# Kernel optimization log

Hardware: AMD Instinct MI355X
Metric: run time of the kernel (lower is better)

## Reference

```python
import jax, jax.numpy as jnp
import numpy as np

N_NODES = 100000
HIDDEN = 128
N_EDGES = 1000000


def setup_inputs() -> dict:
    key = jax.random.key(0)
    k1, k2, k3 = jax.random.split(key, 3)
    z = jax.random.normal(k1, (N_NODES, HIDDEN), dtype=jnp.float32)
    edge_index = jax.random.randint(k2, (2, N_EDGES), 0, N_NODES, dtype=jnp.int64)
    # xavier_uniform for square matrix: bound = sqrt(6/(fan_in+fan_out))
    bound = float(np.sqrt(6.0 / (HIDDEN + HIDDEN)))
    weights = jax.random.uniform(k3, (HIDDEN, HIDDEN), dtype=jnp.float32,
                                 minval=-bound, maxval=bound)
    return {"z": z, "edge_index": edge_index, "weights": weights}


def reference(z, edge_index, weights):
    # symm=True: symmetrize the bilinear form
    W = weights + weights.T                      # [d, d]
    z_src = z[edge_index[0]]                     # [E, d] gather
    z_dst = z[edge_index[1]]                     # [E, d] gather
    # torch: (W @ z_dst.T).T == z_dst @ W.T
    value = jnp.einsum('ed,dk,ek->e', z_src, W, z_dst)  # row-wise bilinear score
    return jax.nn.sigmoid(value)
```

## Files before the change

### kernel.cpp

```cpp
#include <hip/hip_runtime.h>

#define HIDDEN 128
#define BSHIFT 10
#define NBMAX 128
#define CAP 10752

typedef _Float16 f16;
typedef f16 f16x2 __attribute__((ext_vector_type(2)));
typedef f16 f16x4 __attribute__((ext_vector_type(4)));
typedef f16 f16x8 __attribute__((ext_vector_type(8)));
typedef float f32x16 __attribute__((ext_vector_type(16)));
typedef unsigned long long ull;
typedef ull ull2 __attribute__((ext_vector_type(2)));

static __device__ __forceinline__ float fdot2(f16x2 a, f16x2 b, float c) {
    return __builtin_amdgcn_fdot2(a, b, c, false);
}

static __device__ __forceinline__ int widx(int j, int x) {
    return j * HIDDEN + ((((x >> 3) + (j & 7)) & 15) << 3) + (x & 7);
}

static __device__ __forceinline__ void build_w(f16* wlt, const float* __restrict__ w) {
    int tid = threadIdx.x;
    #pragma unroll 4
    for (int it = 0; it < 16; ++it) {
        int idx4 = it * 256 + tid;
        int n = idx4 >> 5, k0 = (idx4 & 31) * 4;
        float4 wv = *(const float4*)&w[n * HIDDEN + k0];
        f16x4 v = {(f16)wv.x, (f16)wv.y, (f16)wv.z, (f16)wv.w};
        *(f16x4*)&wlt[widx(n, k0)] = v;
    }
    __syncthreads();
    for (int kk = 0; kk < 33; ++kk) {
        int i = kk * 256 + tid;
        if (i < 8256) {
            int k = i >> 7, r = i & 127;
            if (k == 0) {
                int e = widx(r, r);
                f16 a = wlt[e];
                wlt[e] = a + a;
            } else {
                int c = (r + k) & 127;
                int ea = widx(r, c), eb = widx(c, r);
                f16 a = wlt[ea], b = wlt[eb];
                f16 s = a + b;
                wlt[ea] = s; wlt[eb] = s;
            }
        }
    }
    __syncthreads();
}

__global__ __launch_bounds__(256, 4) void gemm_scatter(const float* __restrict__ z,
                                                       const float* __restrict__ w,
                                                       f16* __restrict__ zh,
                                                       f16* __restrict__ uh,
                                                       const int* __restrict__ eidx,
                                                       int* __restrict__ cursor,
                                                       ull* __restrict__ perm,
                                                       int nrows, int E, int nb, int ngemm) {
    __shared__ f16 wlt[HIDDEN * HIDDEN];
    int tid = threadIdx.x;

    if (blockIdx.x >= ngemm) {
        int* lh    = (int*)wlt;
        int* lbase = lh + NBMAX;
        int base = (blockIdx.x - ngemm) * 4096;
        if (tid < NBMAX) lh[tid] = 0;
        __syncthreads();
        int s[16], d[16], bb[16];
        #pragma unroll
        for (int i = 0; i < 16; ++i) {
            int e = base + i * 256 + tid;
            bb[i] = -1;
            if (e < E) {
                s[i] = eidx[e]; d[i] = eidx[E + e];
                int b = d[i] >> BSHIFT;
                int r = atomicAdd(&lh[b], 1);
                bb[i] = b | (r << 7);
            }
        }
        __syncthreads();
        if (tid < nb && lh[tid]) lbase[tid] = atomicAdd(&cursor[tid], lh[tid]);
        __syncthreads();
        #pragma unroll
        for (int i = 0; i < 16; ++i) {
            if (bb[i] >= 0) {
                int e = base + i * 256 + tid;
                int b = bb[i] & 127, r = bb[i] >> 7;
                unsigned pib = ((unsigned)(lbase[b] + r)) % CAP;
                ull v = (ull)s[i] | ((ull)d[i] << 17) | ((ull)(e + 1) << 34);
                perm[(long)b * CAP + pib] = v;
            }
        }
        return;
    }

    build_w(wlt, w);

    int wave = tid >> 6, lane = tid & 63;
    int row0 = blockIdx.x * 128 + wave * 32;
    if (row0 > nrows - 32) row0 = nrows - 32;

    int m = lane & 31, half = lane >> 5;
    int rot = m & 7;
    const float* zr = z  + (size_t)(row0 + m) * HIDDEN + half * 8;
    f16*        zhr = zh + (size_t)(row0 + m) * HIDDEN + half * 8;
    const f16* wrow = &wlt[m * HIDDEN];

    f32x16 acc0, acc1, acc2, acc3;
    #pragma unroll
    for (int r = 0; r < 16; ++r) { acc0[r] = 0.f; acc1[r] = 0.f; acc2[r] = 0.f; acc3[r] = 0.f; }

    #pragma unroll
    for (int ks = 0; ks < 8; ++ks) {
        float4 a0 = *(const float4*)(zr + 16 * ks);
        float4 a1 = *(const float4*)(zr + 16 * ks + 4);
        f16x8 af = {(f16)a0.x, (f16)a0.y, (f16)a0.z, (f16)a0.w,
                    (f16)a1.x, (f16)a1.y, (f16)a1.z, (f16)a1.w};
        *(f16x8*)(zhr + 16 * ks) = af;
        int c = ((half + 2 * ks + rot) & 15) << 3;
        f16x8 b0 = *(const f16x8*)&wrow[c];
        f16x8 b1 = *(const f16x8*)&wrow[32 * HIDDEN + c];
        f16x8 b2 = *(const f16x8*)&wrow[64 * HIDDEN + c];
        f16x8 b3 = *(const f16x8*)&wrow[96 * HIDDEN + c];
        acc0 = __builtin_amdgcn_mfma_f32_32x32x16_f16(af, b0, acc0, 0, 0, 0);
        acc1 = __builtin_amdgcn_mfma_f32_32x32x16_f16(af, b1, acc1, 0, 0, 0);
        acc2 = __builtin_amdgcn_mfma_f32_32x32x16_f16(af, b2, acc2, 0, 0, 0);
        acc3 = __builtin_amdgcn_mfma_f32_32x32x16_f16(af, b3, acc3, 0, 0, 0);
    }

    f16* ur = uh + (size_t)row0 * HIDDEN;
    #pragma unroll
    for (int r = 0; r < 16; ++r) {
        int row = (r & 3) + 8 * (r >> 2) + 4 * half;
        f16* p = ur + (size_t)row * HIDDEN + m;
        p[0]  = (f16)acc0[r];
        p[32] = (f16)acc1[r];
        p[64] = (f16)acc2[r];
        p[96] = (f16)acc3[r];
    }
}

static __device__ __forceinline__ void score_edge(const f16* uh, const f16* zh,
                                                  ull p, float* out, int t, int E) {
    int src = (int)(p & 0x1FFFF);
    int dst = (int)((p >> 17) & 0x1FFFF);
    int ep  = (int)(p >> 34);
    const float4* a4 = (const float4*)(uh + (size_t)src * HIDDEN);
    const float4* b4 = (const float4*)(zh + (size_t)dst * HIDDEN);
    float4 av = a4[t], bv = b4[t];
    const f16x2* ap = (const f16x2*)&av;
    const f16x2* bp = (const f16x2*)&bv;
    float s = 0.f;
    #pragma unroll
    for (int i = 0; i < 4; ++i) s = fdot2(ap[i], bp[i], s);
    #pragma unroll
    for (int off = 8; off > 0; off >>= 1) s += __shfl_down(s, off, 16);
    if (t == 0 && ep > 0 && ep <= E) out[ep - 1] = 1.0f / (1.0f + __expf(-s));
}

__global__ __launch_bounds__(256, 8) void edge_bin(const f16* __restrict__ uh,
                                                   const f16* __restrict__ zh,
                                                   const ull* __restrict__ perm,
                                                   float* __restrict__ out,
                                                   int E, int cpx) {
    int tid = threadIdx.x;
    int g = tid >> 4, t = tid & 15;
    int b = blockIdx.x;
    int chunk = (b & 7) * cpx + (b >> 3);
    long slot = (long)chunk * 32 + g * 2;
    ull2 p = *(const ull2*)&perm[slot];

    int src0 = (int)(p.x & 0x1FFFF), dst0 = (int)((p.x >> 17) & 0x1FFFF), e0 = (int)(p.x >> 34);
    int src1 = (int)(p.y & 0x1FFFF), dst1 = (int)((p.y >> 17) & 0x1FFFF), e1 = (int)(p.y >> 34);

    float4 a0 = ((const float4*)(uh + (size_t)src0 * HIDDEN))[t];
    float4 b0 = ((const float4*)(zh + (size_t)dst0 * HIDDEN))[t];
    float4 a1 = ((const float4*)(uh + (size_t)src1 * HIDDEN))[t];
    float4 b1 = ((const float4*)(zh + (size_t)dst1 * HIDDEN))[t];

    const f16x2* ap0 = (const f16x2*)&a0; const f16x2* bp0 = (const f16x2*)&b0;
    const f16x2* ap1 = (const f16x2*)&a1; const f16x2* bp1 = (const f16x2*)&b1;
    float s0 = 0.f, s1 = 0.f;
    #pragma unroll
    for (int i = 0; i < 4; ++i) {
        s0 = fdot2(ap0[i], bp0[i], s0);
        s1 = fdot2(ap1[i], bp1[i], s1);
    }
    #pragma unroll
    for (int off = 8; off > 0; off >>= 1) {
        s0 += __shfl_xor(s0, off, 16);
        s1 += __shfl_xor(s1, off, 16);
    }
    float sv = (t == 0) ? s0 : s1;
    int   ev = (t == 0) ? e0 : e1;
    if (t < 2 && ev > 0 && ev <= E) out[ev - 1] = 1.0f / (1.0f + __expf(-sv));
}

__global__ __launch_bounds__(256, 4) void gemm_only(const float* __restrict__ z,
                                                    const float* __restrict__ w,
                                                    f16* __restrict__ zh,
                                                    f16* __restrict__ uh, int nrows) {
    __shared__ f16 wlt[HIDDEN * HIDDEN];
    int tid = threadIdx.x;
    build_w(wlt, w);

    int wave = tid >> 6, lane = tid & 63;
    int row0 = blockIdx.x * 128 + wave * 32;
    if (row0 > nrows - 32) row0 = nrows - 32;
    int m = lane & 31, half = lane >> 5;
    int rot = m & 7;
    const float* zr = z  + (size_t)(row0 + m) * HIDDEN + half * 8;
    f16*        zhr = zh + (size_t)(row0 + m) * HIDDEN + half * 8;
    const f16* wrow = &wlt[m * HIDDEN];
    f32x16 acc0, acc1, acc2, acc3;
    #pragma unroll
    for (int r = 0; r < 16; ++r) { acc0[r] = 0.f; acc1[r] = 0.f; acc2[r] = 0.f; acc3[r] = 0.f; }
    #pragma unroll
    for (int ks = 0; ks < 8; ++ks) {
        float4 a0 = *(const float4*)(zr + 16 * ks);
        float4 a1 = *(const float4*)(zr + 16 * ks + 4);
        f16x8 af = {(f16)a0.x, (f16)a0.y, (f16)a0.z, (f16)a0.w,
                    (f16)a1.x, (f16)a1.y, (f16)a1.z, (f16)a1.w};
        *(f16x8*)(zhr + 16 * ks) = af;
        int c = ((half + 2 * ks + rot) & 15) << 3;
        f16x8 b0 = *(const f16x8*)&wrow[c];
        f16x8 b1 = *(const f16x8*)&wrow[32 * HIDDEN + c];
        f16x8 b2 = *(const f16x8*)&wrow[64 * HIDDEN + c];
        f16x8 b3 = *(const f16x8*)&wrow[96 * HIDDEN + c];
        acc0 = __builtin_amdgcn_mfma_f32_32x32x16_f16(af, b0, acc0, 0, 0, 0);
        acc1 = __builtin_amdgcn_mfma_f32_32x32x16_f16(af, b1, acc1, 0, 0, 0);
        acc2 = __builtin_amdgcn_mfma_f32_32x32x16_f16(af, b2, acc2, 0, 0, 0);
        acc3 = __builtin_amdgcn_mfma_f32_32x32x16_f16(af, b3, acc3, 0, 0, 0);
    }
    f16* ur = uh + (size_t)row0 * HIDDEN;
    #pragma unroll
    for (int r = 0; r < 16; ++r) {
        int row = (r & 3) + 8 * (r >> 2) + 4 * half;
        f16* p = ur + (size_t)row * HIDDEN + m;
        p[0]  = (f16)acc0[r];
        p[32] = (f16)acc1[r];
        p[64] = (f16)acc2[r];
        p[96] = (f16)acc3[r];
    }
}

__global__ __launch_bounds__(256) void edge_score16(const f16* __restrict__ uh,
                                                    const f16* __restrict__ zh,
                                                    const int* __restrict__ eidx,
                                                    float* __restrict__ out, int E) {
    int tid = threadIdx.x;
    int g = tid >> 4, t = tid & 15;
    int e = blockIdx.x * 16 + g;
    if (e >= E) return;
    ull p = (ull)eidx[e] | ((ull)eidx[E + e] << 17) | ((ull)(e + 1) << 34);
    score_edge(uh, zh, p, out, t, E);
}

extern "C" void kernel_launch(void* const* d_in, const int* in_sizes, int n_in,
                              void* d_out, int out_size, void* d_ws, size_t ws_size,
                              hipStream_t stream) {
    const float* z    = (const float*)d_in[0];
    const int*   eidx = (const int*)d_in[1];
    const float* w    = (const float*)d_in[2];
    float* out = (float*)d_out;

    int nrows = in_sizes[0] / HIDDEN;
    int E = out_size;
    int nb = (nrows >> BSHIFT) + 1;

    f16* zh     = (f16*)d_ws;
    f16* uh     = zh + (size_t)nrows * HIDDEN;
    int* cursor = (int*)(uh + (size_t)nrows * HIDDEN);
    ull* perm   = (ull*)(cursor + NBMAX + 4);

    long nslots = (long)nb * CAP;
    size_t need = (size_t)((char*)(perm + nslots) - (char*)d_ws);
    bool binned = ws_size >= need;

    int ngemm = (nrows + 127) / 128;
    int nscat = (E + 4095) / 4096;

    if (binned) {
        gemm_scatter<<<ngemm + nscat, 256, 0, stream>>>(z, w, zh, uh, eidx, cursor,
                                                        perm, nrows, E, nb, ngemm);
        long ngrp = nslots / 32;
        int cpx = (int)(ngrp / 8);
        edge_bin<<<(int)ngrp, 256, 0, stream>>>(uh, zh, perm, out, E, cpx);
    } else {
        gemm_only<<<ngemm, 256, 0, stream>>>(z, w, zh, uh, nrows);
        edge_score16<<<(E + 15) / 16, 256, 0, stream>>>(uh, zh, eidx, out, E);
    }
}
```

Measured before the change: 161.4 us.

## Precompute symmetrized fp16 W in a prep kernel and process two row tiles per block

A small prep kernel now builds the symmetrized, transposed fp16 weight matrix once into workspace. GEMM blocks copy it into LDS with vectorized loads instead of each block redoing the symmetrization with two barrier phases. Each GEMM block also handles 256 rows (two 128-row tiles), which halves the GEMM block count and spreads the W setup cost over more rows. The price is one extra kernel launch and fewer GEMM blocks for parallelism.

```diff
diff --git a/kernel.cpp b/kernel.cpp
--- a/kernel.cpp
+++ b/kernel.cpp
@@ -7,7 +7,6 @@
 
 typedef _Float16 f16;
 typedef f16 f16x2 __attribute__((ext_vector_type(2)));
-typedef f16 f16x4 __attribute__((ext_vector_type(4)));
 typedef f16 f16x8 __attribute__((ext_vector_type(8)));
 typedef float f32x16 __attribute__((ext_vector_type(16)));
 typedef unsigned long long ull;
@@ -17,43 +16,15 @@
     return __builtin_amdgcn_fdot2(a, b, c, false);
 }
 
-static __device__ __forceinline__ int widx(int j, int x) {
-    return j * HIDDEN + ((((x >> 3) + (j & 7)) & 15) << 3) + (x & 7);
-}
-
-static __device__ __forceinline__ void build_w(f16* wlt, const float* __restrict__ w) {
-    int tid = threadIdx.x;
-    #pragma unroll 4
-    for (int it = 0; it < 16; ++it) {
-        int idx4 = it * 256 + tid;
-        int n = idx4 >> 5, k0 = (idx4 & 31) * 4;
-        float4 wv = *(const float4*)&w[n * HIDDEN + k0];
-        f16x4 v = {(f16)wv.x, (f16)wv.y, (f16)wv.z, (f16)wv.w};
-        *(f16x4*)&wlt[widx(n, k0)] = v;
-    }
-    __syncthreads();
-    for (int kk = 0; kk < 33; ++kk) {
-        int i = kk * 256 + tid;
-        if (i < 8256) {
-            int k = i >> 7, r = i & 127;
-            if (k == 0) {
-                int e = widx(r, r);
-                f16 a = wlt[e];
-                wlt[e] = a + a;
-            } else {
-                int c = (r + k) & 127;
-                int ea = widx(r, c), eb = widx(c, r);
-                f16 a = wlt[ea], b = wlt[eb];
-                f16 s = a + b;
-                wlt[ea] = s; wlt[eb] = s;
-            }
-        }
-    }
-    __syncthreads();
+__global__ __launch_bounds__(256) void prep_w(const float* __restrict__ w,
+                                              f16* __restrict__ wsh_t) {
+    int idx = blockIdx.x * 256 + threadIdx.x;
+    int n = idx >> 7, k = idx & 127;
+    wsh_t[idx] = (f16)(w[k * HIDDEN + n] + w[n * HIDDEN + k]);
 }
 
 __global__ __launch_bounds__(256, 4) void gemm_scatter(const float* __restrict__ z,
-                                                       const float* __restrict__ w,
+                                                       const f16* __restrict__ wsh_t,
                                                        f16* __restrict__ zh,
                                                        f16* __restrict__ uh,
                                                        const int* __restrict__ eidx,
@@ -97,49 +68,62 @@
         return;
     }
 
-    build_w(wlt, w);
+    {
+        const f16x8* g = (const f16x8*)wsh_t;
+        #pragma unroll
+        for (int it = 0; it < 8; ++it) {
+            int idx = it * 256 + tid;
+            int j = idx >> 4, kc = idx & 15;
+            *(f16x8*)&wlt[j * HIDDEN + (((kc + (j & 7)) & 15) << 3)] = g[idx];
+        }
+    }
+    __syncthreads();
 
     int wave = tid >> 6, lane = tid & 63;
-    int row0 = blockIdx.x * 128 + wave * 32;
-    if (row0 > nrows - 32) row0 = nrows - 32;
-
     int m = lane & 31, half = lane >> 5;
     int rot = m & 7;
-    const float* zr = z  + (size_t)(row0 + m) * HIDDEN + half * 8;
-    f16*        zhr = zh + (size_t)(row0 + m) * HIDDEN + half * 8;
     const f16* wrow = &wlt[m * HIDDEN];
 
-    f32x16 acc0, acc1, acc2, acc3;
-    #pragma unroll
-    for (int r = 0; r < 16; ++r) { acc0[r] = 0.f; acc1[r] = 0.f; acc2[r] = 0.f; acc3[r] = 0.f; }
-
-    #pragma unroll
-    for (int ks = 0; ks < 8; ++ks) {
-        float4 a0 = *(const float4*)(zr + 16 * ks);
-        float4 a1 = *(const float4*)(zr + 16 * ks + 4);
-        f16x8 af = {(f16)a0.x, (f16)a0.y, (f16)a0.z, (f16)a0.w,
-                    (f16)a1.x, (f16)a1.y, (f16)a1.z, (f16)a1.w};
-        *(f16x8*)(zhr + 16 * ks) = af;
-        int c = ((half + 2 * ks + rot) & 15) << 3;
-        f16x8 b0 = *(const f16x8*)&wrow[c];
-        f16x8 b1 = *(const f16x8*)&wrow[32 * HIDDEN + c];
-        f16x8 b2 = *(const f16x8*)&wrow[64 * HIDDEN + c];
-        f16x8 b3 = *(const f16x8*)&wrow[96 * HIDDEN + c];
-        acc0 = __builtin_amdgcn_mfma_f32_32x32x16_f16(af, b0, acc0, 0, 0, 0);
-        acc1 = __builtin_amdgcn_mfma_f32_32x32x16_f16(af, b1, acc1, 0, 0, 0);
-        acc2 = __builtin_amdgcn_mfma_f32_32x32x16_f16(af, b2, acc2, 0, 0, 0);
-        acc3 = __builtin_amdgcn_mfma_f32_32x32x16_f16(af, b3, acc3, 0, 0, 0);
-    }
-
-    f16* ur = uh + (size_t)row0 * HIDDEN;
-    #pragma unroll
-    for (int r = 0; r < 16; ++r) {
-        int row = (r & 3) + 8 * (r >> 2) + 4 * half;
-        f16* p = ur + (size_t)row * HIDDEN + m;
-        p[0]  = (f16)acc0[r];
-        p[32] = (f16)acc1[r];
-        p[64] = (f16)acc2[r];
-        p[96] = (f16)acc3[r];
+    #pragma unroll
+    for (int t = 0; t < 2; ++t) {
+        int row0 = blockIdx.x * 256 + t * 128 + wave * 32;
+        if (row0 > nrows - 32) row0 = nrows - 32;
+
+        const float* zr = z  + (size_t)(row0 + m) * HIDDEN + half * 8;
+        f16*        zhr = zh + (size_t)(row0 + m) * HIDDEN + half * 8;
+
+        f32x16 acc0, acc1, acc2, acc3;
+        #pragma unroll
+        for (int r = 0; r < 16; ++r) { acc0[r] = 0.f; acc1[r] = 0.f; acc2[r] = 0.f; acc3[r] = 0.f; }
+
+        #pragma unroll
+        for (int ks = 0; ks < 8; ++ks) {
+            float4 a0 = *(const float4*)(zr + 16 * ks);
+            float4 a1 = *(const float4*)(zr + 16 * ks + 4);
+            f16x8 af = {(f16)a0.x, (f16)a0.y, (f16)a0.z, (f16)a0.w,
+                        (f16)a1.x, (f16)a1.y, (f16)a1.z, (f16)a1.w};
+            *(f16x8*)(zhr + 16 * ks) = af;
+            int c = ((half + 2 * ks + rot) & 15) << 3;
+            f16x8 b0 = *(const f16x8*)&wrow[c];
+            f16x8 b1 = *(const f16x8*)&wrow[32 * HIDDEN + c];
+            f16x8 b2 = *(const f16x8*)&wrow[64 * HIDDEN + c];
+            f16x8 b3 = *(const f16x8*)&wrow[96 * HIDDEN + c];
+            acc0 = __builtin_amdgcn_mfma_f32_32x32x16_f16(af, b0, acc0, 0, 0, 0);
+            acc1 = __builtin_amdgcn_mfma_f32_32x32x16_f16(af, b1, acc1, 0, 0, 0);
+            acc2 = __builtin_amdgcn_mfma_f32_32x32x16_f16(af, b2, acc2, 0, 0, 0);
+            acc3 = __builtin_amdgcn_mfma_f32_32x32x16_f16(af, b3, acc3, 0, 0, 0);
+        }
+
+        f16* ur = uh + (size_t)row0 * HIDDEN;
+        #pragma unroll
+        for (int r = 0; r < 16; ++r) {
+            int row = (r & 3) + 8 * (r >> 2) + 4 * half;
+            f16* p = ur + (size_t)row * HIDDEN + m;
+            p[0]  = (f16)acc0[r];
+            p[32] = (f16)acc1[r];
+            p[64] = (f16)acc2[r];
+            p[96] = (f16)acc3[r];
+        }
     }
 }
 
@@ -200,50 +184,62 @@
 }
 
 __global__ __launch_bounds__(256, 4) void gemm_only(const float* __restrict__ z,
-                                                    const float* __restrict__ w,
+                                                    const f16* __restrict__ wsh_t,
                                                     f16* __restrict__ zh,
                                                     f16* __restrict__ uh, int nrows) {
     __shared__ f16 wlt[HIDDEN * HIDDEN];
     int tid = threadIdx.x;
-    build_w(wlt, w);
+    {
+        const f16x8* g = (const f16x8*)wsh_t;
+        #pragma unroll
+        for (int it = 0; it < 8; ++it) {
+            int idx = it * 256 + tid;
+            int j = idx >> 4, kc = idx & 15;
+            *(f16x8*)&wlt[j * HIDDEN + (((kc + (j & 7)) & 15) << 3)] = g[idx];
+        }
+    }
+    __syncthreads();
 
     int wave = tid >> 6, lane = tid & 63;
-    int row0 = blockIdx.x * 128 + wave * 32;
-    if (row0 > nrows - 32) row0 = nrows - 32;
     int m = lane & 31, half = lane >> 5;
     int rot = m & 7;
-    const float* zr = z  + (size_t)(row0 + m) * HIDDEN + half * 8;
-    f16*        zhr = zh + (size_t)(row0 + m) * HIDDEN + half * 8;
     const f16* wrow = &wlt[m * HIDDEN];
-    f32x16 acc0, acc1, acc2, acc3;
-    #pragma unroll
-    for (int r = 0; r < 16; ++r) { acc0[r] = 0.f; acc1[r] = 0.f; acc2[r] = 0.f; acc3[r] = 0.f; }
-    #pragma unroll
-    for (int ks = 0; ks < 8; ++ks) {
-        float4 a0 = *(const float4*)(zr + 16 * ks);
-        float4 a1 = *(const float4*)(zr + 16 * ks + 4);
-        f16x8 af = {(f16)a0.x, (f16)a0.y, (f16)a0.z, (f16)a0.w,
-                    (f16)a1.x, (f16)a1.y, (f16)a1.z, (f16)a1.w};
-        *(f16x8*)(zhr + 16 * ks) = af;
-        int c = ((half + 2 * ks + rot) & 15) << 3;
-        f16x8 b0 = *(const f16x8*)&wrow[c];
-        f16x8 b1 = *(const f16x8*)&wrow[32 * HIDDEN + c];
-        f16x8 b2 = *(const f16x8*)&wrow[64 * HIDDEN + c];
-        f16x8 b3 = *(const f16x8*)&wrow[96 * HIDDEN + c];
-        acc0 = __builtin_amdgcn_mfma_f32_32x32x16_f16(af, b0, acc0, 0, 0, 0);
-        acc1 = __builtin_amdgcn_mfma_f32_32x32x16_f16(af, b1, acc1, 0, 0, 0);
-        acc2 = __builtin_amdgcn_mfma_f32_32x32x16_f16(af, b2, acc2, 0, 0, 0);
-        acc3 = __builtin_amdgcn_mfma_f32_32x32x16_f16(af, b3, acc3, 0, 0, 0);
-    }
-    f16* ur = uh + (size_t)row0 * HIDDEN;
-    #pragma unroll
-    for (int r = 0; r < 16; ++r) {
-        int row = (r & 3) + 8 * (r >> 2) + 4 * half;
-        f16* p = ur + (size_t)row * HIDDEN + m;
-        p[0]  = (f16)acc0[r];
-        p[32] = (f16)acc1[r];
-        p[64] = (f16)acc2[r];
-        p[96] = (f16)acc3[r];
+    #pragma unroll
+    for (int t = 0; t < 2; ++t) {
+        int row0 = blockIdx.x * 256 + t * 128 + wave * 32;
+        if (row0 > nrows - 32) row0 = nrows - 32;
+        const float* zr = z  + (size_t)(row0 + m) * HIDDEN + half * 8;
+        f16*        zhr = zh + (size_t)(row0 + m) * HIDDEN + half * 8;
+        f32x16 acc0, acc1, acc2, acc3;
+        #pragma unroll
+        for (int r = 0; r < 16; ++r) { acc0[r] = 0.f; acc1[r] = 0.f; acc2[r] = 0.f; acc3[r] = 0.f; }
+        #pragma unroll
+        for (int ks = 0; ks < 8; ++ks) {
+            float4 a0 = *(const float4*)(zr + 16 * ks);
+            float4 a1 = *(const float4*)(zr + 16 * ks + 4);
+            f16x8 af = {(f16)a0.x, (f16)a0.y, (f16)a0.z, (f16)a0.w,
+                        (f16)a1.x, (f16)a1.y, (f16)a1.z, (f16)a1.w};
+            *(f16x8*)(zhr + 16 * ks) = af;
+            int c = ((half + 2 * ks + rot) & 15) << 3;
+            f16x8 b0 = *(const f16x8*)&wrow[c];
+            f16x8 b1 = *(const f16x8*)&wrow[32 * HIDDEN + c];
+            f16x8 b2 = *(const f16x8*)&wrow[64 * HIDDEN + c];
+            f16x8 b3 = *(const f16x8*)&wrow[96 * HIDDEN + c];
+            acc0 = __builtin_amdgcn_mfma_f32_32x32x16_f16(af, b0, acc0, 0, 0, 0);
+            acc1 = __builtin_amdgcn_mfma_f32_32x32x16_f16(af, b1, acc1, 0, 0, 0);
+            acc2 = __builtin_amdgcn_mfma_f32_32x32x16_f16(af, b2, acc2, 0, 0, 0);
+            acc3 = __builtin_amdgcn_mfma_f32_32x32x16_f16(af, b3, acc3, 0, 0, 0);
+        }
+        f16* ur = uh + (size_t)row0 * HIDDEN;
+        #pragma unroll
+        for (int r = 0; r < 16; ++r) {
+            int row = (r & 3) + 8 * (r >> 2) + 4 * half;
+            f16* p = ur + (size_t)row * HIDDEN + m;
+            p[0]  = (f16)acc0[r];
+            p[32] = (f16)acc1[r];
+            p[64] = (f16)acc2[r];
+            p[96] = (f16)acc3[r];
+        }
     }
 }
 
@@ -271,7 +267,8 @@
     int E = out_size;
     int nb = (nrows >> BSHIFT) + 1;
 
-    f16* zh     = (f16*)d_ws;
+    f16* wsh_t  = (f16*)d_ws;
+    f16* zh     = wsh_t + HIDDEN * HIDDEN;
     f16* uh     = zh + (size_t)nrows * HIDDEN;
     int* cursor = (int*)(uh + (size_t)nrows * HIDDEN);
     ull* perm   = (ull*)(cursor + NBMAX + 4);
@@ -280,17 +277,18 @@
     size_t need = (size_t)((char*)(perm + nslots) - (char*)d_ws);
     bool binned = ws_size >= need;
 
-    int ngemm = (nrows + 127) / 128;
+    int ngemm = (nrows + 255) / 256;
     int nscat = (E + 4095) / 4096;
 
+    prep_w<<<64, 256, 0, stream>>>(w, wsh_t);
     if (binned) {
-        gemm_scatter<<<ngemm + nscat, 256, 0, stream>>>(z, w, zh, uh, eidx, cursor,
+        gemm_scatter<<<ngemm + nscat, 256, 0, stream>>>(z, wsh_t, zh, uh, eidx, cursor,
                                                         perm, nrows, E, nb, ngemm);
         long ngrp = nslots / 32;
         int cpx = (int)(ngrp / 8);
         edge_bin<<<(int)ngrp, 256, 0, stream>>>(uh, zh, perm, out, E, cpx);
     } else {
-        gemm_only<<<ngemm, 256, 0, stream>>>(z, w, zh, uh, nrows);
+        gemm_only<<<ngemm, 256, 0, stream>>>(z, wsh_t, zh, uh, nrows);
         edge_score16<<<(E + 15) / 16, 256, 0, stream>>>(uh, zh, eidx, out, E);
     }
 }
```

Measured after the change: 167.2 us. 1.04x slower.
